# Optimization experiments

Hardware: AMD Instinct MI355X
Metric: run time of the kernel (lower is better)

The kernel has to match this reference:

```python
import jax, jax.numpy as jnp
import numpy as np

N0, N1 = 30000, 20000
N = N0 + N1
E = 400000
H0, H1, H2 = 4, 4, 1
DH = 64            # num_hidden
NC = 16            # num_classes
IN = 128           # per-type input feature dim
SLOPE = 0.2        # leaky relu negative slope


def setup_inputs() -> dict:
    key = jax.random.key(0)
    ks = iter(jax.random.split(key, 48))
    rn = lambda shape, s=0.05: jax.random.normal(next(ks), shape, jnp.float32) * s
    ri = lambda shape: jax.random.randint(next(ks), shape, 0, N, jnp.int32)
    inp = {
        'features0': rn((N0, IN), 1.0),
        'features1': rn((N1, IN), 1.0),
        'fc_w0': rn((IN, DH)), 'fc_b0': jnp.zeros((DH,), jnp.float32),
        'fc_w1': rn((IN, DH)), 'fc_b1': jnp.zeros((DH,), jnp.float32),
        'mix_w': jnp.zeros((2, 3, 2), jnp.float32),  # (n_types, num_layers+1, n_graphs)
        # GATConv params stacked over the 2 relation graphs
        'W0': rn((2, DH, H0 * DH)), 'al0': rn((2, H0, DH), 0.1), 'ar0': rn((2, H0, DH), 0.1), 'b0': jnp.zeros((2, H0 * DH), jnp.float32),
        'W1': rn((2, H0 * DH, H1 * DH)), 'al1': rn((2, H1, DH), 0.1), 'ar1': rn((2, H1, DH), 0.1), 'b1': jnp.zeros((2, H1 * DH), jnp.float32),
        'W2': rn((2, H1 * DH, H2 * NC)), 'al2': rn((2, H2, NC), 0.1), 'ar2': rn((2, H2, NC), 0.1), 'b2': jnp.zeros((2, H2 * NC), jnp.float32),
        'res2': rn((2, H1 * DH, H2 * NC)),  # res_fc for last layer (in != out*heads)
        'src0': ri((E,)), 'dst0': ri((E,)),
        'src1': ri((E,)), 'dst1': ri((E,)),
    }
    return inp


def gat_conv(h, src, dst, W, al, ar, b, H, D, res_mode, res_w, act):
    # h: (N, in)  ->  (N, H, D)
    feat = (h @ W).reshape(N, H, D)
    el = jnp.sum(feat * al, axis=-1)   # (N, H)
    er = jnp.sum(feat * ar, axis=-1)   # (N, H)
    e = jax.nn.leaky_relu(el[src] + er[dst], SLOPE)  # (E, H)
    # edge softmax over incoming edges of each dst node
    m = jax.ops.segment_max(e, dst, num_segments=N)
    ex = jnp.exp(e - m[dst])
    den = jax.ops.segment_sum(ex, dst, num_segments=N)
    alpha = ex / den[dst]                              # (E, H)
    out = jax.ops.segment_sum(feat[src] * alpha[..., None], dst, num_segments=N)
    if res_mode == 'id':
        out = out + h.reshape(N, H, D)
    elif res_mode == 'fc':
        out = out + (h @ res_w).reshape(N, H, D)
    out = out + b.reshape(1, H, D)
    return jax.nn.elu(out) if act else out


def _forward(features0, features1, fc_w0, fc_b0, fc_w1, fc_b1, mix_w,
             W0, al0, ar0, b0, W1, al1, ar1, b1, W2, al2, ar2, b2, res2,
             src0, dst0, src1, dst1):
    nt = jnp.concatenate([jnp.zeros(N0, jnp.int32), jnp.ones(N1, jnp.int32)])
    w = jax.nn.softmax(mix_w, axis=2)  # (types, layers+1, graphs)
    h = jnp.concatenate([features0 @ fc_w0 + fc_b0, features1 @ fc_w1 + fc_b1], axis=0)
    srcs, dsts = (src0, src1), (dst0, dst1)
    layers = [
        (W0, al0, ar0, b0, H0, DH, None, True),
        (W1, al1, ar1, b1, H1, DH, 'id', True),
    ]
    for l, (W, al, ar, b, H, D, rm, act) in enumerate(layers):
        acc = 0.
        for i in range(2):
            o = gat_conv(h, srcs[i], dsts[i], W[i], al[i], ar[i], b[i], H, D, rm, None, act)
            acc = acc + o.reshape(N, H * D) * w[nt, l, i][:, None]
        h = acc
    logits = 0.
    for i in range(2):
        o = gat_conv(h, srcs[i], dsts[i], W2[i], al2[i], ar2[i], b2[i], H2, NC, 'fc', res2[i], False)
        logits = logits + o.mean(axis=1) * w[nt, 2, i][:, None]
    return logits


def reference(features0, features1, fc_w0, fc_b0, fc_w1, fc_b1, mix_w,
              W0, al0, ar0, b0, W1, al1, ar1, b1, W2, al2, ar2, b2, res2,
              src0, dst0, src1, dst1):
    return _forward(features0, features1, fc_w0, fc_b0, fc_w1, fc_b1, mix_w,
                    W0, al0, ar0, b0, W1, al1, ar1, b1, W2, al2, ar2, b2, res2,
                    src0, dst0, src1, dst1)
```

## Files before the change

### kernel.cpp

```cpp
#include <hip/hip_runtime.h>
#include <hip/hip_bf16.h>

#define NN   50000
#define NN0  30000
#define EE   400000
#define NB_SCAN ((NN + 1023) / 1024)
#define NRT   3125
#define NGRP  ((NRT + 3) / 4)
#define NT0   1875

typedef unsigned short u16;
typedef unsigned int   u32;

typedef __attribute__((ext_vector_type(8))) __bf16 bf16x8;
typedef __attribute__((ext_vector_type(4))) float  f32x4;

__device__ __forceinline__ float bf2f(u16 u){ return __uint_as_float(((u32)u)<<16); }
__device__ __forceinline__ float lo16(u32 u){ return __uint_as_float(u<<16); }
__device__ __forceinline__ float hi16(u32 u){ return __uint_as_float(u & 0xffff0000u); }
__device__ __forceinline__ u16 f2bf(float f){
  u32 x = __float_as_uint(f);
  x += 0x7fffu + ((x>>16)&1u);
  return (u16)(x>>16);
}
__device__ __forceinline__ float elu_f(float x){ return x>0.f ? x : __expf(x)-1.f; }
__device__ __forceinline__ float lrelu(float x){ return x>0.f ? x : 0.2f*x; }
__device__ __forceinline__ bf16x8 ld_frag(const u16* p){
  uint4 v = *(const uint4*)p;
  return __builtin_bit_cast(bf16x8, v);
}
__device__ __forceinline__ bf16x8 cvt8(const float* p){
  float4 u = ((const float4*)p)[0];
  float4 v = ((const float4*)p)[1];
  u32 w0 = (u32)f2bf(u.x) | ((u32)f2bf(u.y)<<16);
  u32 w1 = (u32)f2bf(u.z) | ((u32)f2bf(u.w)<<16);
  u32 w2 = (u32)f2bf(v.x) | ((u32)f2bf(v.y)<<16);
  u32 w3 = (u32)f2bf(v.z) | ((u32)f2bf(v.w)<<16);
  uint4 r{w0,w1,w2,w3};
  return __builtin_bit_cast(bf16x8, r);
}

__global__ __launch_bounds__(256) void k_prep(
    const float* __restrict__ mix_w, float* __restrict__ wsoft,
    const float* __restrict__ W0, u16* __restrict__ W0p,
    const float* __restrict__ W1, u16* __restrict__ W1p,
    const float* __restrict__ W2, const float* __restrict__ res2, u16* __restrict__ W2p,
    const float* __restrict__ fcw0, const float* __restrict__ fcw1, u16* __restrict__ Fp,
    const float* __restrict__ al0, const float* __restrict__ ar0, u16* __restrict__ Vp)
{
  int t = blockIdx.x*256 + threadIdx.x;
  if (t < 6){
    float a0 = mix_w[t*2+0], a1 = mix_w[t*2+1];
    float mx = fmaxf(a0,a1);
    float e0 = __expf(a0-mx), e1 = __expf(a1-mx);
    wsoft[t*2+0] = e0/(e0+e1); wsoft[t*2+1] = e1/(e0+e1);
  }
  if (t < 4096){
    int gg = t>>11, fi = t&2047;
    int lane = fi&63, kb = (fi>>6)&1, ct = fi>>7;
    int q = lane>>4, c = lane&15;
    const float* src = W0 + (size_t)gg*16384;
    u16* o = W0p + (size_t)gg*16384 + (size_t)fi*8;
    #pragma unroll
    for (int j=0;j<8;j++) o[j] = f2bf(src[(size_t)(kb*32+q*8+j)*256 + ct*16 + c]);
  } else if (t < 20480){
    int u = t - 4096;
    int gg = u>>13, fi = u&8191;
    int lane = fi&63, kb = (fi>>6)&7, ct = fi>>9;
    int q = lane>>4, c = lane&15;
    const float* src = W1 + (size_t)gg*65536;
    u16* o = W1p + (size_t)gg*65536 + (size_t)fi*8;
    #pragma unroll
    for (int j=0;j<8;j++) o[j] = f2bf(src[(size_t)(kb*32+q*8+j)*256 + ct*16 + c]);
  } else if (t < 22528){
    int fi = t - 20480;
    int lane = fi&63, kb = (fi>>6)&7, ct = fi>>9;
    int q = lane>>4, c = lane&15;
    int cl = ct*16 + c;
    int i = cl>>5, which = (cl>>4)&1;
    const float* src = which ? res2 : W2;
    u16* o = W2p + (size_t)fi*8;
    #pragma unroll
    for (int j=0;j<8;j++) o[j] = f2bf(src[(size_t)i*4096 + (size_t)(kb*32+q*8+j)*16 + (cl&15)]);
  } else if (t < 24576){
    int u = t - 22528;
    int tt = u>>10, fi = u&1023;
    int lane = fi&63, kb = (fi>>6)&3, ct = fi>>8;
    int q = lane>>4, c = lane&15;
    const float* src = tt ? fcw1 : fcw0;
    u16* o = Fp + (size_t)tt*8192 + (size_t)fi*8;
    #pragma unroll
    for (int j=0;j<8;j++) o[j] = f2bf(src[(size_t)(kb*32+q*8+j)*64 + ct*16 + c]);
  } else if (t < 25600){
    int u = t - 24576;
    int fi = u>>3, j = u&7;
    int lane = fi&63, kb = fi>>6;
    int q = lane>>4, c = lane&15;
    int k = kb*32 + q*8 + j;
    int which = c>>3, g=(c>>2)&1, h=c&3;
    const float* sel = (which ? ar0 : al0) + (size_t)(g*4+h)*64;
    const float* Wrow = W0 + (size_t)g*16384 + (size_t)k*256 + h*64;
    float s=0.f;
    #pragma unroll 8
    for (int d=0;d<64;d++) s = fmaf(Wrow[d], sel[d], s);
    Vp[(size_t)fi*8 + j] = f2bf(s);
  }
}

__global__ void k_count2(const int* __restrict__ d0, const int* __restrict__ d1,
                         int* __restrict__ cnt2){
  int t = blockIdx.x*256 + threadIdx.x;
  int g = blockIdx.y;
  if (t < EE) atomicAdd(&cnt2[g*NN + (g ? d1[t] : d0[t])], 1);
}

__global__ __launch_bounds__(1024) void k_scan1(const int* __restrict__ cnt2,
                                                int* __restrict__ row2, int* __restrict__ bsum){
  __shared__ int wsum[16];
  int g = blockIdx.y;
  int lane = threadIdx.x & 63, wid = threadIdx.x >> 6;
  int i = blockIdx.x*1024 + threadIdx.x;
  int v = (i < NN) ? cnt2[g*NN + i] : 0;
  int x = v;
  #pragma unroll
  for (int off = 1; off < 64; off <<= 1){
    int y = __shfl_up(x, off, 64);
    if (lane >= off) x += y;
  }
  if (lane == 63) wsum[wid] = x;
  __syncthreads();
  if (wid == 0 && lane < 16){
    int s = wsum[lane];
    #pragma unroll
    for (int off = 1; off < 16; off <<= 1){
      int y = __shfl_up(s, off, 16);
      if (lane >= off) s += y;
    }
    wsum[lane] = s;
  }
  __syncthreads();
  int incl = x + (wid ? wsum[wid-1] : 0);
  if (i < NN) row2[(size_t)g*(NN+1) + i] = incl - v;
  if (threadIdx.x == 1023) bsum[g*NB_SCAN + blockIdx.x] = incl;
}

__global__ __launch_bounds__(128) void k_scan2(const int* __restrict__ bsum, int* __restrict__ boff){
  int g = threadIdx.x >> 6, lane = threadIdx.x & 63;
  int v = (lane < NB_SCAN) ? bsum[g*NB_SCAN + lane] : 0;
  int x = v;
  #pragma unroll
  for (int off = 1; off < 64; off <<= 1){
    int y = __shfl_up(x, off, 64);
    if (lane >= off) x += y;
  }
  if (lane < NB_SCAN) boff[g*NB_SCAN + lane] = x - v;
}

__global__ __launch_bounds__(1024) void k_scan3(int* __restrict__ row2, const int* __restrict__ boff){
  int g = blockIdx.y;
  int i = blockIdx.x*1024 + threadIdx.x;
  if (i < NN) row2[(size_t)g*(NN+1) + i] += boff[g*NB_SCAN + blockIdx.x];
  if (blockIdx.x == 0 && threadIdx.x == 0) row2[(size_t)g*(NN+1) + NN] = EE;
}

__global__ void k_scatter2(const int* __restrict__ s0, const int* __restrict__ d0,
                           const int* __restrict__ s1, const int* __restrict__ d1,
                           const int* __restrict__ row2, int* __restrict__ fill2,
                           int* __restrict__ col2){
  int t = blockIdx.x*256 + threadIdx.x;
  int g = blockIdx.y;
  if (t >= EE) return;
  int d = g ? d1[t] : d0[t];
  int s = g ? s1[t] : s0[t];
  int pos = atomicAdd(&fill2[g*NN + d], 1);
  col2[(size_t)g*EE + row2[(size_t)g*(NN+1) + d] + pos] = s;
}

__global__ __launch_bounds__(256) void k_inproj_m(
    const float* __restrict__ f0, const float* __restrict__ f1,
    const u16* __restrict__ Fp, const float* __restrict__ fb0, const float* __restrict__ fb1,
    u16* __restrict__ h0)
{
  int wv = threadIdx.x>>6, ln = threadIdx.x&63;
  int ti = blockIdx.x*4 + wv;
  if (ti >= NRT) return;
  int q = ln>>4, c = ln&15;
  int type = (ti < NT0) ? 0 : 1;
  const float* F = type ? f1 : f0;
  int rbase = type ? (ti*16 - NN0) : ti*16;
  const u16* Bg = Fp + (size_t)type*8192;
  const float* bb = type ? fb1 : fb0;
  f32x4 acc[4] = {};
  const float* Ap = F + (size_t)(rbase + c)*128;
  #pragma unroll
  for (int kb=0; kb<4; kb++){
    bf16x8 a = cvt8(Ap + kb*32 + q*8);
    #pragma unroll
    for (int ct=0; ct<4; ct++){
      bf16x8 b = ld_frag(Bg + ((size_t)(ct*4+kb)*64 + ln)*8);
      acc[ct] = __builtin_amdgcn_mfma_f32_16x16x32_bf16(a, b, acc[ct], 0,0,0);
    }
  }
  #pragma unroll
  for (int ct=0; ct<4; ct++){
    float bv = bb[ct*16+c];
    #pragma unroll
    for (int j=0;j<4;j++){
      int row = ti*16 + q*4 + j;
      h0[(size_t)row*64 + ct*16 + c] = f2bf(acc[ct][j] + bv);
    }
  }
}

__global__ __launch_bounds__(256) void k_eler0(
    const u16* __restrict__ h0, const u16* __restrict__ Vp,
    float* __restrict__ elA, float* __restrict__ erA)
{
  int wv = threadIdx.x>>6, ln = threadIdx.x&63;
  int ti = blockIdx.x*4 + wv;
  if (ti >= NRT) return;
  int q = ln>>4, c = ln&15;
  f32x4 acc = {};
  const u16* Ap = h0 + (size_t)(ti*16 + c)*64 + q*8;
  #pragma unroll
  for (int kb=0; kb<2; kb++){
    bf16x8 a = ld_frag(Ap + kb*32);
    bf16x8 b = ld_frag(Vp + ((size_t)(kb*64 + ln))*8);
    acc = __builtin_amdgcn_mfma_f32_16x16x32_bf16(a, b, acc, 0,0,0);
  }
  int which = c>>3, g = (c>>2)&1, h = c&3;
  float* dst = (which ? erA : elA) + (size_t)g*NN*4;
  #pragma unroll
  for (int j=0;j<4;j++){
    int row = ti*16 + q*4 + j;
    dst[row*4 + h] = acc[j];
  }
}

__global__ __launch_bounds__(256) void k_agg0(
    const int* __restrict__ row2, const int* __restrict__ col2,
    const u16* __restrict__ h0,
    const float* __restrict__ elA, const float* __restrict__ erA,
    u16* __restrict__ aggB, size_t aggStride)
{
  int wv = threadIdx.x>>6, ln = threadIdx.x&63;
  int n = blockIdx.x*4 + wv;
  #pragma unroll
  for (int g=0; g<2; g++){
    const int* rw = row2 + (size_t)g*(NN+1);
    const int* cl = col2 + (size_t)g*EE;
    const float* elg = elA + (size_t)g*NN*4;
    float4 er4 = ((const float4*)(erA + (size_t)g*NN*4))[n];
    int beg = rw[n], end = rw[n+1];
    float d0=0.f,d1=0.f,d2=0.f,d3=0.f;
    float a0=0.f,a1=0.f,a2=0.f,a3=0.f;
    int k = beg;
    for (; k+2<=end; k+=2){
      int s0 = cl[k], s1 = cl[k+1];
      float4 e0 = ((const float4*)elg)[s0];
      float4 e1 = ((const float4*)elg)[s1];
      float v0 = bf2f(h0[(size_t)s0*64 + ln]);
      float v1 = bf2f(h0[(size_t)s1*64 + ln]);
      float x00=__expf(lrelu(e0.x+er4.x)), x01=__expf(lrelu(e0.y+er4.y));
      float x02=__expf(lrelu(e0.z+er4.z)), x03=__expf(lrelu(e0.w+er4.w));
      float x10=__expf(lrelu(e1.x+er4.x)), x11=__expf(lrelu(e1.y+er4.y));
      float x12=__expf(lrelu(e1.z+er4.z)), x13=__expf(lrelu(e1.w+er4.w));
      d0 += x00+x10; d1 += x01+x11; d2 += x02+x12; d3 += x03+x13;
      a0 += x00*v0 + x10*v1; a1 += x01*v0 + x11*v1;
      a2 += x02*v0 + x12*v1; a3 += x03*v0 + x13*v1;
    }
    for (; k<end; k++){
      int s = cl[k];
      float4 e0 = ((const float4*)elg)[s];
      float v = bf2f(h0[(size_t)s*64 + ln]);
      float x0=__expf(lrelu(e0.x+er4.x)), x1=__expf(lrelu(e0.y+er4.y));
      float x2=__expf(lrelu(e0.z+er4.z)), x3=__expf(lrelu(e0.w+er4.w));
      d0+=x0; d1+=x1; d2+=x2; d3+=x3;
      a0+=x0*v; a1+=x1*v; a2+=x2*v; a3+=x3*v;
    }
    bool has = (end > beg);
    a0 = has ? a0/d0 : 0.f; a1 = has ? a1/d1 : 0.f;
    a2 = has ? a2/d2 : 0.f; a3 = has ? a3/d3 : 0.f;
    u16* og = aggB + (size_t)g*aggStride + (size_t)n*256 + ln;
    og[0]   = f2bf(a0); og[64]  = f2bf(a1);
    og[128] = f2bf(a2); og[192] = f2bf(a3);
  }
}

__global__ __launch_bounds__(256) void k_head0(
    const u16* __restrict__ aggB, size_t aggStride,
    const u16* __restrict__ W0p, const float* __restrict__ b0,
    const float* __restrict__ wsoft, u16* __restrict__ h1)
{
  int wv = threadIdx.x>>6, ln = threadIdx.x&63;
  int ti = blockIdx.x*4 + wv;
  if (ti >= NRT) return;
  int q = ln>>4, c = ln&15;
  int type = (ti < NT0) ? 0 : 1;
  float wg0 = wsoft[type*6 + 0];
  float wg1 = wsoft[type*6 + 1];
  for (int h=0; h<4; h++){
    f32x4 acc[2][4] = {};
    #pragma unroll
    for (int g=0; g<2; g++){
      const u16* Ap = aggB + (size_t)g*aggStride + (size_t)(ti*16 + c)*256 + h*64 + q*8;
      const u16* Bg = W0p + (size_t)g*16384;
      #pragma unroll
      for (int kb=0; kb<2; kb++){
        bf16x8 a = ld_frag(Ap + kb*32);
        #pragma unroll
        for (int ct=0; ct<4; ct++){
          int ctg = h*4 + ct;
          bf16x8 b = ld_frag(Bg + ((size_t)(ctg*2 + kb)*64 + ln)*8);
          acc[g][ct] = __builtin_amdgcn_mfma_f32_16x16x32_bf16(a, b, acc[g][ct], 0,0,0);
        }
      }
    }
    #pragma unroll
    for (int ct=0; ct<4; ct++){
      int colg = h*64 + ct*16 + c;
      float bb0 = b0[colg], bb1 = b0[256 + colg];
      #pragma unroll
      for (int j=0;j<4;j++){
        int row = ti*16 + q*4 + j;
        float o = wg0*elu_f(acc[0][ct][j] + bb0) + wg1*elu_f(acc[1][ct][j] + bb1);
        h1[(size_t)row*256 + colg] = f2bf(o);
      }
    }
  }
}

template<int K>
__global__ __launch_bounds__(256) void k_gemm4(
    const u16* __restrict__ A,
    const u16* __restrict__ Bp, size_t bpStride,
    const float* __restrict__ al, const float* __restrict__ ar, int alStride,
    u16* __restrict__ feat, size_t featStride,
    float* __restrict__ el, float* __restrict__ er, size_t elStride)
{
  constexpr int KB = K/32;
  int wv = threadIdx.x>>6, ln = threadIdx.x&63;
  int bid = blockIdx.x;
  int g = bid / NGRP, grp = bid % NGRP;
  int split = wv, q = ln>>4, c = ln&15;
  const u16* Bpg = Bp + (size_t)g*bpStride;
  const float* alg = al + (size_t)g*alStride;
  const float* arg = ar + (size_t)g*alStride;
  u16* featg = feat + (size_t)g*featStride;
  float* elg = el + (size_t)g*elStride;
  float* erg = er + (size_t)g*elStride;

  f32x4 acc[4][4] = {};
  int  tbase = grp*4;
  bool valid[4];
  const u16* Ap[4];
  #pragma unroll
  for (int rt=0; rt<4; rt++){
    int ti = tbase + rt;
    valid[rt] = (ti < NRT);
    if (!valid[rt]) ti = NRT-1;
    Ap[rt] = A + (size_t)(ti*16 + c)*K + q*8;
  }
  const u16* Bbase = Bpg + ((size_t)(split*4)*KB*64 + ln)*8;

  #pragma unroll 2
  for (int kb=0; kb<KB; kb++){
    bf16x8 b[4], a[4];
    #pragma unroll
    for (int ct=0; ct<4; ct++) b[ct] = ld_frag(Bbase + (size_t)(ct*KB + kb)*64*8);
    #pragma unroll
    for (int rt=0; rt<4; rt++) a[rt] = ld_frag(Ap[rt] + kb*32);
    #pragma unroll
    for (int rt=0; rt<4; rt++)
      #pragma unroll
      for (int ct=0; ct<4; ct++)
        acc[rt][ct] = __builtin_amdgcn_mfma_f32_16x16x32_bf16(a[rt], b[ct], acc[rt][ct], 0,0,0);
  }

  float alv[4], arv[4];
  #pragma unroll
  for (int ct=0;ct<4;ct++){
    int cg = (split*4+ct)*16 + c;
    alv[ct] = alg[cg]; arv[ct] = arg[cg];
  }
  #pragma unroll
  for (int rt=0; rt<4; rt++){
    if (!valid[rt]) continue;
    int row0 = (tbase+rt)*16;
    #pragma unroll
    for (int j=0;j<4;j++){
      float ep=0.f, rp=0.f;
      #pragma unroll
      for (int ct=0;ct<4;ct++){ ep += acc[rt][ct][j]*alv[ct]; rp += acc[rt][ct][j]*arv[ct]; }
      #pragma unroll
      for (int off=8; off; off>>=1){ ep += __shfl_xor(ep,off,16); rp += __shfl_xor(rp,off,16); }
      int row = row0 + q*4 + j;
      if (c==0){ elg[row*4+split]=ep; erg[row*4+split]=rp; }
      #pragma unroll
      for (int ct=0;ct<4;ct++)
        featg[(size_t)row*256 + (split*4+ct)*16 + c] = f2bf(acc[rt][ct][j]);
    }
  }
}

template<int RES>
__global__ __launch_bounds__(256) void k_aggNF(
    const int* __restrict__ row2, const int* __restrict__ col2,
    const u16* __restrict__ feat, size_t featStride,
    const float* __restrict__ el, const float* __restrict__ er, size_t elStride,
    const u16* __restrict__ hres, const float* __restrict__ bias,
    const float* __restrict__ wsoft, int l,
    u16* __restrict__ hout)
{
  int wv = threadIdx.x>>6, ln = threadIdx.x&63;
  int n = blockIdx.x*4 + wv;
  int h = ln>>4;
  int type = (n<NN0)?0:1;
  float rx=0.f, ry=0.f, rz=0.f, rw_=0.f;
  if (RES){
    uint2 r = ((const uint2*)hres)[(size_t)n*64 + ln];
    rx=lo16(r.x); ry=hi16(r.x); rz=lo16(r.y); rw_=hi16(r.y);
  }
  float o0=0.f,o1=0.f,o2=0.f,o3=0.f;
  #pragma unroll
  for (int g=0; g<2; g++){
    const int* rw = row2 + (size_t)g*(NN+1);
    const int* cl = col2 + (size_t)g*EE;
    const uint2* fp = (const uint2*)(feat + (size_t)g*featStride);
    const float* elg = el + (size_t)g*elStride;
    float er_h = (er + (size_t)g*elStride)[n*4+h];
    int beg = rw[n], end = rw[n+1];
    float den = 0.f;
    float a0=0.f,a1=0.f,a2=0.f,a3=0.f;
    int k = beg;
    for (; k+4<=end; k+=4){
      int s0=cl[k], s1=cl[k+1], s2=cl[k+2], s3=cl[k+3];
      float x0 = __expf(lrelu(elg[s0*4+h] + er_h));
      float x1 = __expf(lrelu(elg[s1*4+h] + er_h));
      float x2 = __expf(lrelu(elg[s2*4+h] + er_h));
      float x3 = __expf(lrelu(elg[s3*4+h] + er_h));
      uint2 f0 = fp[(size_t)s0*64 + ln];
      uint2 f1 = fp[(size_t)s1*64 + ln];
      uint2 f2 = fp[(size_t)s2*64 + ln];
      uint2 f3 = fp[(size_t)s3*64 + ln];
      den += (x0+x1) + (x2+x3);
      a0 += x0*lo16(f0.x) + x1*lo16(f1.x) + x2*lo16(f2.x) + x3*lo16(f3.x);
      a1 += x0*hi16(f0.x) + x1*hi16(f1.x) + x2*hi16(f2.x) + x3*hi16(f3.x);
      a2 += x0*lo16(f0.y) + x1*lo16(f1.y) + x2*lo16(f2.y) + x3*lo16(f3.y);
      a3 += x0*hi16(f0.y) + x1*hi16(f1.y) + x2*hi16(f2.y) + x3*hi16(f3.y);
    }
    for (; k<end; k++){
      int s = cl[k];
      float x = __expf(lrelu(elg[s*4+h] + er_h));
      uint2 f = fp[(size_t)s*64 + ln];
      den += x;
      a0 += x*lo16(f.x); a1 += x*hi16(f.x); a2 += x*lo16(f.y); a3 += x*hi16(f.y);
    }
    float inv = (end>beg) ? 1.0f/den : 0.f;
    float4 bv = ((const float4*)(bias + g*256))[ln];
    a0 = a0*inv + bv.x; a1 = a1*inv + bv.y; a2 = a2*inv + bv.z; a3 = a3*inv + bv.w;
    if (RES){ a0 += rx; a1 += ry; a2 += rz; a3 += rw_; }
    float w = wsoft[type*6 + l*2 + g];
    o0 += w*elu_f(a0); o1 += w*elu_f(a1); o2 += w*elu_f(a2); o3 += w*elu_f(a3);
  }
  uint2 o;
  o.x = (u32)f2bf(o0) | ((u32)f2bf(o1)<<16);
  o.y = (u32)f2bf(o2) | ((u32)f2bf(o3)<<16);
  ((uint2*)hout)[(size_t)n*64 + ln] = o;
}

__global__ __launch_bounds__(256) void k_gemm2(
    const u16* __restrict__ A, const u16* __restrict__ Bp,
    const float* __restrict__ al2, const float* __restrict__ ar2,
    float* __restrict__ feat16, float* __restrict__ resb,
    float* __restrict__ el2, float* __restrict__ er2)
{
  int wv = threadIdx.x>>6, ln = threadIdx.x&63;
  int wt = blockIdx.x*4 + wv;
  if (wt >= NRT) return;
  int row0 = wt*16;
  int q = ln>>4, c = ln&15;
  f32x4 acc[4] = {};
  const u16* Ap = A + (size_t)(row0 + c)*256 + q*8;
  #pragma unroll
  for (int kb=0; kb<8; kb++){
    bf16x8 a = ld_frag(Ap + kb*32);
    #pragma unroll
    for (int t=0;t<4;t++){
      bf16x8 b = ld_frag(Bp + ((size_t)(t*8 + kb)*64 + ln)*8);
      acc[t] = __builtin_amdgcn_mfma_f32_16x16x32_bf16(a, b, acc[t], 0,0,0);
    }
  }
  #pragma unroll
  for (int i=0;i<2;i++){
    float alv = al2[i*16+c], arv = ar2[i*16+c];
    #pragma unroll
    for (int j=0;j<4;j++){
      float ep = acc[2*i][j]*alv, rp = acc[2*i][j]*arv;
      #pragma unroll
      for (int off=8; off; off>>=1){ ep += __shfl_xor(ep,off,16); rp += __shfl_xor(rp,off,16); }
      if (c==0){
        int row = row0 + q*4 + j;
        el2[(size_t)i*NN + row] = ep; er2[(size_t)i*NN + row] = rp;
      }
    }
    #pragma unroll
    for (int j=0;j<4;j++){
      int row = row0 + q*4 + j;
      feat16[(size_t)i*NN*16 + (size_t)row*16 + c] = acc[2*i][j];
      resb  [(size_t)i*NN*16 + (size_t)row*16 + c] = acc[2*i+1][j];
    }
  }
}

__global__ __launch_bounds__(256) void k_agg2D(
    const int* __restrict__ row2, const int* __restrict__ col2,
    const float* __restrict__ feat16, const float* __restrict__ el2,
    const float* __restrict__ er2, const float* __restrict__ resb,
    const float* __restrict__ b2, const float* __restrict__ wsoft,
    float* __restrict__ out)
{
  int t = threadIdx.x;
  int nl = t>>4, j = t&15;
  int n = blockIdx.x*16 + nl;
  int type = (n<NN0)?0:1;
  float o = 0.f;
  #pragma unroll
  for (int i=0;i<2;i++){
    const int* rw = row2 + (size_t)i*(NN+1);
    const int* cl = col2 + (size_t)i*EE;
    const float* f  = feat16 + (size_t)i*NN*16;
    const float* eli= el2 + (size_t)i*NN;
    float ern = er2[(size_t)i*NN + n];
    int beg = rw[n], end = rw[n+1];
    float den = 0.f, acc = 0.f;
    int k = beg;
    for (; k+4<=end; k+=4){
      int s0=cl[k], s1=cl[k+1], s2=cl[k+2], s3=cl[k+3];
      float x0 = __expf(lrelu(eli[s0] + ern));
      float x1 = __expf(lrelu(eli[s1] + ern));
      float x2 = __expf(lrelu(eli[s2] + ern));
      float x3 = __expf(lrelu(eli[s3] + ern));
      float v0 = f[(size_t)s0*16 + j];
      float v1 = f[(size_t)s1*16 + j];
      float v2 = f[(size_t)s2*16 + j];
      float v3 = f[(size_t)s3*16 + j];
      den += (x0+x1) + (x2+x3);
      acc += x0*v0 + x1*v1 + x2*v2 + x3*v3;
    }
    for (; k<end; k++){
      int s = cl[k];
      float x = __expf(lrelu(eli[s] + ern));
      den += x;
      acc = fmaf(x, f[(size_t)s*16 + j], acc);
    }
    float inv = (end>beg) ? 1.0f/den : 0.f;
    float oi = acc*inv + b2[i*16+j] + resb[(size_t)i*NN*16 + (size_t)n*16 + j];
    o += oi * wsoft[type*6 + 4 + i];
  }
  out[(size_t)n*16 + j] = o;
}

extern "C" void kernel_launch(void* const* d_in, const int* in_sizes, int n_in,
                              void* d_out, int out_size, void* d_ws, size_t ws_size,
                              hipStream_t stream)
{
  const float* features0 = (const float*)d_in[0];
  const float* features1 = (const float*)d_in[1];
  const float* fc_w0 = (const float*)d_in[2];
  const float* fc_b0 = (const float*)d_in[3];
  const float* fc_w1 = (const float*)d_in[4];
  const float* fc_b1 = (const float*)d_in[5];
  const float* mix_w = (const float*)d_in[6];
  const float* W0  = (const float*)d_in[7];
  const float* al0 = (const float*)d_in[8];
  const float* ar0 = (const float*)d_in[9];
  const float* b0  = (const float*)d_in[10];
  const float* W1  = (const float*)d_in[11];
  const float* al1 = (const float*)d_in[12];
  const float* ar1 = (const float*)d_in[13];
  const float* b1  = (const float*)d_in[14];
  const float* W2  = (const float*)d_in[15];
  const float* al2 = (const float*)d_in[16];
  const float* ar2 = (const float*)d_in[17];
  const float* b2  = (const float*)d_in[18];
  const float* res2= (const float*)d_in[19];
  const int* src[2] = {(const int*)d_in[20], (const int*)d_in[22]};
  const int* dst[2] = {(const int*)d_in[21], (const int*)d_in[23]};
  (void)in_sizes; (void)n_in; (void)out_size; (void)ws_size;

  char* ws = (char*)d_ws;
  size_t off = 0;
  auto alloc = [&](size_t bytes)->char*{
    char* p = ws + off; off += (bytes + 255) & ~(size_t)255; return p;
  };
  float* wsoft = (float*)alloc(64*4);
  u16*   W0p   = (u16*)  alloc((size_t)2*64*256*2);
  u16*   W1p   = (u16*)  alloc((size_t)2*256*256*2);
  u16*   W2p   = (u16*)  alloc((size_t)256*64*2);
  u16*   Fp    = (u16*)  alloc((size_t)2*128*64*2);
  u16*   Vp    = (u16*)  alloc((size_t)64*16*2);
  int*   row2  = (int*)  alloc((size_t)2*(NN+1)*4);
  int*   col2  = (int*)  alloc((size_t)2*EE*4);
  int*   zeros = (int*)  alloc((size_t)4*NN*4);
  int*   cnt2  = zeros;
  int*   fill2 = zeros + 2*NN;
  int*   bsum  = (int*)alloc((size_t)2*NB_SCAN*4);
  int*   boff  = (int*)alloc((size_t)2*NB_SCAN*4);
  u16*   h0    = (u16*)alloc((size_t)NN*64*2);
  u16*   h1    = (u16*)alloc((size_t)NN*256*2);
  u16*   h2    = (u16*)alloc((size_t)NN*256*2);
  float* elA   = (float*)alloc((size_t)2*NN*4*4);
  float* erA   = (float*)alloc((size_t)2*NN*4*4);
  size_t featStride = (size_t)NN*256;
  size_t off_D = off;
  u16* regionD = (u16*)alloc(2*featStride*2);
  u16* aggB  = regionD;
  u16* featD = regionD;
  float* feat16 = (float*)(ws + off_D);
  float* resb   = feat16 + (size_t)2*NN*16;
  float* el2    = resb   + (size_t)2*NN*16;
  float* er2    = el2    + (size_t)2*NN;

  k_prep<<<100,256,0,stream>>>(mix_w, wsoft, W0, W0p, W1, W1p, W2, res2, W2p,
                               fc_w0, fc_w1, Fp, al0, ar0, Vp);

  hipMemsetAsync(zeros, 0, (size_t)4*NN*4, stream);
  {
    dim3 gE((EE+255)/256, 2), gS(NB_SCAN, 2);
    k_count2 <<<gE,256,0,stream>>>(dst[0], dst[1], cnt2);
    k_scan1  <<<gS,1024,0,stream>>>(cnt2, row2, bsum);
    k_scan2  <<<1,128,0,stream>>>(bsum, boff);
    k_scan3  <<<gS,1024,0,stream>>>(row2, boff);
    k_scatter2<<<gE,256,0,stream>>>(src[0], dst[0], src[1], dst[1], row2, fill2, col2);
  }

  k_inproj_m<<<NGRP,256,0,stream>>>(features0, features1, Fp, fc_b0, fc_b1, h0);
  k_eler0   <<<NGRP,256,0,stream>>>(h0, Vp, elA, erA);

  k_agg0 <<<NN/4,256,0,stream>>>(row2, col2, h0, elA, erA, aggB, featStride);
  k_head0<<<NGRP,256,0,stream>>>(aggB, featStride, W0p, b0, wsoft, h1);

  k_gemm4<256><<<2*NGRP,256,0,stream>>>(h1, W1p, (size_t)256*256, al1, ar1, 256,
                                        featD, featStride, elA, erA, (size_t)NN*4);
  k_aggNF<1><<<NN/4,256,0,stream>>>(row2, col2, featD, featStride, elA, erA, (size_t)NN*4,
                                    h1, b1, wsoft, 1, h2);

  k_gemm2<<<NGRP,256,0,stream>>>(h2, W2p, al2, ar2, feat16, resb, el2, er2);
  k_agg2D<<<NN/16,256,0,stream>>>(row2, col2, feat16, el2, er2, resb, b2, wsoft, (float*)d_out);
}
```

Measured before the change: 465.9 us.

## Precompute per-edge attention exponentials in CSR order and shrink column indices to u16

Measured after the change: 459.5 us. About the same (-1.4%).

```diff
diff --git a/kernel.cpp b/kernel.cpp
--- a/kernel.cpp
+++ b/kernel.cpp
@@ -166,14 +166,47 @@
 __global__ void k_scatter2(const int* __restrict__ s0, const int* __restrict__ d0,
                            const int* __restrict__ s1, const int* __restrict__ d1,
                            const int* __restrict__ row2, int* __restrict__ fill2,
-                           int* __restrict__ col2){
+                           u16* __restrict__ col2, u16* __restrict__ dstOf){
   int t = blockIdx.x*256 + threadIdx.x;
   int g = blockIdx.y;
   if (t >= EE) return;
   int d = g ? d1[t] : d0[t];
   int s = g ? s1[t] : s0[t];
   int pos = atomicAdd(&fill2[g*NN + d], 1);
-  col2[(size_t)g*EE + row2[(size_t)g*(NN+1) + d] + pos] = s;
+  size_t slot = (size_t)g*EE + row2[(size_t)g*(NN+1) + d] + pos;
+  col2[slot]  = (u16)s;
+  dstOf[slot] = (u16)d;
+}
+
+__global__ void k_alpha4(const u16* __restrict__ col2, const u16* __restrict__ dstOf,
+                         const float* __restrict__ el, const float* __restrict__ er,
+                         size_t elStride, float* __restrict__ xbuf){
+  int t = blockIdx.x*256 + threadIdx.x;
+  int g = blockIdx.y;
+  if (t >= EE) return;
+  size_t slot = (size_t)g*EE + t;
+  int s = col2[slot], d = dstOf[slot];
+  const float* elg = el + (size_t)g*elStride;
+  const float* erg = er + (size_t)g*elStride;
+  float4 e4 = ((const float4*)elg)[s];
+  float4 r4 = ((const float4*)erg)[d];
+  float4 x;
+  x.x = __expf(lrelu(e4.x + r4.x));
+  x.y = __expf(lrelu(e4.y + r4.y));
+  x.z = __expf(lrelu(e4.z + r4.z));
+  x.w = __expf(lrelu(e4.w + r4.w));
+  ((float4*)xbuf)[slot] = x;
+}
+
+__global__ void k_alpha1(const u16* __restrict__ col2, const u16* __restrict__ dstOf,
+                         const float* __restrict__ el2, const float* __restrict__ er2,
+                         float* __restrict__ xb2){
+  int t = blockIdx.x*256 + threadIdx.x;
+  int g = blockIdx.y;
+  if (t >= EE) return;
+  size_t slot = (size_t)g*EE + t;
+  int s = col2[slot], d = dstOf[slot];
+  xb2[slot] = __expf(lrelu(el2[(size_t)g*NN + s] + er2[(size_t)g*NN + d]));
 }
 
 __global__ __launch_bounds__(256) void k_inproj_m(
@@ -238,9 +271,8 @@
 }
 
 __global__ __launch_bounds__(256) void k_agg0(
-    const int* __restrict__ row2, const int* __restrict__ col2,
-    const u16* __restrict__ h0,
-    const float* __restrict__ elA, const float* __restrict__ erA,
+    const int* __restrict__ row2, const u16* __restrict__ col2,
+    const float* __restrict__ xbuf, const u16* __restrict__ h0,
     u16* __restrict__ aggB, size_t aggStride)
 {
   int wv = threadIdx.x>>6, ln = threadIdx.x&63;
@@ -248,35 +280,27 @@
   #pragma unroll
   for (int g=0; g<2; g++){
     const int* rw = row2 + (size_t)g*(NN+1);
-    const int* cl = col2 + (size_t)g*EE;
-    const float* elg = elA + (size_t)g*NN*4;
-    float4 er4 = ((const float4*)(erA + (size_t)g*NN*4))[n];
+    const u16* cl = col2 + (size_t)g*EE;
+    const float4* xb = (const float4*)xbuf + (size_t)g*EE;
     int beg = rw[n], end = rw[n+1];
     float d0=0.f,d1=0.f,d2=0.f,d3=0.f;
     float a0=0.f,a1=0.f,a2=0.f,a3=0.f;
     int k = beg;
     for (; k+2<=end; k+=2){
       int s0 = cl[k], s1 = cl[k+1];
-      float4 e0 = ((const float4*)elg)[s0];
-      float4 e1 = ((const float4*)elg)[s1];
+      float4 x0 = xb[k], x1 = xb[k+1];
       float v0 = bf2f(h0[(size_t)s0*64 + ln]);
       float v1 = bf2f(h0[(size_t)s1*64 + ln]);
-      float x00=__expf(lrelu(e0.x+er4.x)), x01=__expf(lrelu(e0.y+er4.y));
-      float x02=__expf(lrelu(e0.z+er4.z)), x03=__expf(lrelu(e0.w+er4.w));
-      float x10=__expf(lrelu(e1.x+er4.x)), x11=__expf(lrelu(e1.y+er4.y));
-      float x12=__expf(lrelu(e1.z+er4.z)), x13=__expf(lrelu(e1.w+er4.w));
-      d0 += x00+x10; d1 += x01+x11; d2 += x02+x12; d3 += x03+x13;
-      a0 += x00*v0 + x10*v1; a1 += x01*v0 + x11*v1;
-      a2 += x02*v0 + x12*v1; a3 += x03*v0 + x13*v1;
+      d0 += x0.x+x1.x; d1 += x0.y+x1.y; d2 += x0.z+x1.z; d3 += x0.w+x1.w;
+      a0 += x0.x*v0 + x1.x*v1; a1 += x0.y*v0 + x1.y*v1;
+      a2 += x0.z*v0 + x1.z*v1; a3 += x0.w*v0 + x1.w*v1;
     }
     for (; k<end; k++){
       int s = cl[k];
-      float4 e0 = ((const float4*)elg)[s];
+      float4 x = xb[k];
       float v = bf2f(h0[(size_t)s*64 + ln]);
-      float x0=__expf(lrelu(e0.x+er4.x)), x1=__expf(lrelu(e0.y+er4.y));
-      float x2=__expf(lrelu(e0.z+er4.z)), x3=__expf(lrelu(e0.w+er4.w));
-      d0+=x0; d1+=x1; d2+=x2; d3+=x3;
-      a0+=x0*v; a1+=x1*v; a2+=x2*v; a3+=x3*v;
+      d0+=x.x; d1+=x.y; d2+=x.z; d3+=x.w;
+      a0+=x.x*v; a1+=x.y*v; a2+=x.z*v; a3+=x.w*v;
     }
     bool has = (end > beg);
     a0 = has ? a0/d0 : 0.f; a1 = has ? a1/d1 : 0.f;
@@ -405,9 +429,9 @@
 
 template<int RES>
 __global__ __launch_bounds__(256) void k_aggNF(
-    const int* __restrict__ row2, const int* __restrict__ col2,
+    const int* __restrict__ row2, const u16* __restrict__ col2,
+    const float* __restrict__ xbuf,
     const u16* __restrict__ feat, size_t featStride,
-    const float* __restrict__ el, const float* __restrict__ er, size_t elStride,
     const u16* __restrict__ hres, const float* __restrict__ bias,
     const float* __restrict__ wsoft, int l,
     u16* __restrict__ hout)
@@ -425,20 +449,19 @@
   #pragma unroll
   for (int g=0; g<2; g++){
     const int* rw = row2 + (size_t)g*(NN+1);
-    const int* cl = col2 + (size_t)g*EE;
+    const u16* cl = col2 + (size_t)g*EE;
+    const float* xb = xbuf + (size_t)g*EE*4;
     const uint2* fp = (const uint2*)(feat + (size_t)g*featStride);
-    const float* elg = el + (size_t)g*elStride;
-    float er_h = (er + (size_t)g*elStride)[n*4+h];
     int beg = rw[n], end = rw[n+1];
     float den = 0.f;
     float a0=0.f,a1=0.f,a2=0.f,a3=0.f;
     int k = beg;
     for (; k+4<=end; k+=4){
       int s0=cl[k], s1=cl[k+1], s2=cl[k+2], s3=cl[k+3];
-      float x0 = __expf(lrelu(elg[s0*4+h] + er_h));
-      float x1 = __expf(lrelu(elg[s1*4+h] + er_h));
-      float x2 = __expf(lrelu(elg[s2*4+h] + er_h));
-      float x3 = __expf(lrelu(elg[s3*4+h] + er_h));
+      float x0 = xb[(size_t)k*4 + h];
+      float x1 = xb[(size_t)(k+1)*4 + h];
+      float x2 = xb[(size_t)(k+2)*4 + h];
+      float x3 = xb[(size_t)(k+3)*4 + h];
       uint2 f0 = fp[(size_t)s0*64 + ln];
       uint2 f1 = fp[(size_t)s1*64 + ln];
       uint2 f2 = fp[(size_t)s2*64 + ln];
@@ -451,7 +474,7 @@
     }
     for (; k<end; k++){
       int s = cl[k];
-      float x = __expf(lrelu(elg[s*4+h] + er_h));
+      float x = xb[(size_t)k*4 + h];
       uint2 f = fp[(size_t)s*64 + ln];
       den += x;
       a0 += x*lo16(f.x); a1 += x*hi16(f.x); a2 += x*lo16(f.y); a3 += x*hi16(f.y);
@@ -514,9 +537,9 @@
 }
 
 __global__ __launch_bounds__(256) void k_agg2D(
-    const int* __restrict__ row2, const int* __restrict__ col2,
-    const float* __restrict__ feat16, const float* __restrict__ el2,
-    const float* __restrict__ er2, const float* __restrict__ resb,
+    const int* __restrict__ row2, const u16* __restrict__ col2,
+    const float* __restrict__ xb2,
+    const float* __restrict__ feat16, const float* __restrict__ resb,
     const float* __restrict__ b2, const float* __restrict__ wsoft,
     float* __restrict__ out)
 {
@@ -528,19 +551,15 @@
   #pragma unroll
   for (int i=0;i<2;i++){
     const int* rw = row2 + (size_t)i*(NN+1);
-    const int* cl = col2 + (size_t)i*EE;
+    const u16* cl = col2 + (size_t)i*EE;
+    const float* xb = xb2 + (size_t)i*EE;
     const float* f  = feat16 + (size_t)i*NN*16;
-    const float* eli= el2 + (size_t)i*NN;
-    float ern = er2[(size_t)i*NN + n];
     int beg = rw[n], end = rw[n+1];
     float den = 0.f, acc = 0.f;
     int k = beg;
     for (; k+4<=end; k+=4){
       int s0=cl[k], s1=cl[k+1], s2=cl[k+2], s3=cl[k+3];
-      float x0 = __expf(lrelu(eli[s0] + ern));
-      float x1 = __expf(lrelu(eli[s1] + ern));
-      float x2 = __expf(lrelu(eli[s2] + ern));
-      float x3 = __expf(lrelu(eli[s3] + ern));
+      float x0 = xb[k], x1 = xb[k+1], x2 = xb[k+2], x3 = xb[k+3];
       float v0 = f[(size_t)s0*16 + j];
       float v1 = f[(size_t)s1*16 + j];
       float v2 = f[(size_t)s2*16 + j];
@@ -550,7 +569,7 @@
     }
     for (; k<end; k++){
       int s = cl[k];
-      float x = __expf(lrelu(eli[s] + ern));
+      float x = xb[k];
       den += x;
       acc = fmaf(x, f[(size_t)s*16 + j], acc);
     }
@@ -601,7 +620,8 @@
   u16*   Fp    = (u16*)  alloc((size_t)2*128*64*2);
   u16*   Vp    = (u16*)  alloc((size_t)64*16*2);
   int*   row2  = (int*)  alloc((size_t)2*(NN+1)*4);
-  int*   col2  = (int*)  alloc((size_t)2*EE*4);
+  u16*   col2  = (u16*)  alloc((size_t)2*EE*2);
+  u16*   dstOf = (u16*)  alloc((size_t)2*EE*2);
   int*   zeros = (int*)  alloc((size_t)4*NN*4);
   int*   cnt2  = zeros;
   int*   fill2 = zeros + 2*NN;
@@ -612,6 +632,7 @@
   u16*   h2    = (u16*)alloc((size_t)NN*256*2);
   float* elA   = (float*)alloc((size_t)2*NN*4*4);
   float* erA   = (float*)alloc((size_t)2*NN*4*4);
+  float* xbuf  = (float*)alloc((size_t)2*EE*4*4);
   size_t featStride = (size_t)NN*256;
   size_t off_D = off;
   u16* regionD = (u16*)alloc(2*featStride*2);
@@ -632,20 +653,25 @@
     k_scan1  <<<gS,1024,0,stream>>>(cnt2, row2, bsum);
     k_scan2  <<<1,128,0,stream>>>(bsum, boff);
     k_scan3  <<<gS,1024,0,stream>>>(row2, boff);
-    k_scatter2<<<gE,256,0,stream>>>(src[0], dst[0], src[1], dst[1], row2, fill2, col2);
+    k_scatter2<<<gE,256,0,stream>>>(src[0], dst[0], src[1], dst[1], row2, fill2, col2, dstOf);
   }
 
   k_inproj_m<<<NGRP,256,0,stream>>>(features0, features1, Fp, fc_b0, fc_b1, h0);
   k_eler0   <<<NGRP,256,0,stream>>>(h0, Vp, elA, erA);
 
-  k_agg0 <<<NN/4,256,0,stream>>>(row2, col2, h0, elA, erA, aggB, featStride);
+  dim3 gE((EE+255)/256, 2);
+
+  k_alpha4<<<gE,256,0,stream>>>(col2, dstOf, elA, erA, (size_t)NN*4, xbuf);
+  k_agg0 <<<NN/4,256,0,stream>>>(row2, col2, xbuf, h0, aggB, featStride);
   k_head0<<<NGRP,256,0,stream>>>(aggB, featStride, W0p, b0, wsoft, h1);
 
   k_gemm4<256><<<2*NGRP,256,0,stream>>>(h1, W1p, (size_t)256*256, al1, ar1, 256,
                                         featD, featStride, elA, erA, (size_t)NN*4);
-  k_aggNF<1><<<NN/4,256,0,stream>>>(row2, col2, featD, featStride, elA, erA, (size_t)NN*4,
+  k_alpha4<<<gE,256,0,stream>>>(col2, dstOf, elA, erA, (size_t)NN*4, xbuf);
+  k_aggNF<1><<<NN/4,256,0,stream>>>(row2, col2, xbuf, featD, featStride,
                                     h1, b1, wsoft, 1, h2);
 
   k_gemm2<<<NGRP,256,0,stream>>>(h2, W2p, al2, ar2, feat16, resb, el2, er2);
-  k_agg2D<<<NN/16,256,0,stream>>>(row2, col2, feat16, el2, er2, resb, b2, wsoft, (float*)d_out);
-}
+  k_alpha1<<<gE,256,0,stream>>>(col2, dstOf, el2, er2, xbuf);
+  k_agg2D<<<NN/16,256,0,stream>>>(row2, col2, xbuf, feat16, resb, b2, wsoft, (float*)d_out);
+}
```
